# Kernel tuning notes

Hardware: AMD Instinct MI355X
Metric: run time of the kernel (lower is better)

Reference implementation:

```python
import jax, jax.numpy as jnp
import numpy as np

B, S, D, H = 8, 512, 768, 12
DH = D // H  # head size 64


def setup_inputs() -> dict:
    key = jax.random.key(0)
    ks = jax.random.split(key, 24)
    std = D ** -0.5
    w = lambda k, shape: jax.random.normal(k, shape, jnp.float32) * std
    b = lambda k, n: jax.random.normal(k, (n,), jnp.float32) * 0.01
    return {
        "hidden_states": jax.random.normal(ks[0], (B, S, D), jnp.float32),
        "mol": jax.random.normal(ks[1], (B, S, D), jnp.float32),
        "Wq": w(ks[2], (D, D)), "bq": b(ks[3], D),
        "Wk": w(ks[4], (D, D)), "bk": b(ks[5], D),
        "Wv": w(ks[6], (D, D)), "bv": b(ks[7], D),
        "Wqm": w(ks[8], (D, D)), "bqm": b(ks[9], D),
        "Wkm": w(ks[10], (D, D)), "bkm": b(ks[11], D),
        "Wvm": w(ks[12], (D, D)), "bvm": b(ks[13], D),
        "Wfc": w(ks[14], (2 * D, D)), "bfc": b(ks[15], D),
        "Wfcm": w(ks[16], (2 * D, D)), "bfcm": b(ks[17], D),
        "Wo": w(ks[18], (D, D)), "bo": b(ks[19], D),
        "Wom": w(ks[20], (D, D)), "bom": b(ks[21], D),
    }


def _split_heads(x):
    # [B,S,D] -> [B,H,S,DH]
    b_, s_, _ = x.shape
    return x.reshape(b_, s_, H, DH).transpose(0, 2, 1, 3)


def _merge_heads(x):
    # [B,H,S,DH] -> [B,S,D]
    b_, _, s_, _ = x.shape
    return x.transpose(0, 2, 1, 3).reshape(b_, s_, H * DH)


def _attend(q, k, v):
    # q:[B,H,Sq,DH], k,v:[B,H,Sk,DH]  (dropout rate = 0 -> identity)
    scores = jnp.einsum('bhqd,bhkd->bhqk', q, k) / np.sqrt(DH).astype(np.float32)
    probs = jax.nn.softmax(scores, axis=-1)
    return _merge_heads(jnp.einsum('bhqk,bhkd->bhqd', probs, v))


def reference(hidden_states, mol, Wq, bq, Wk, bk, Wv, bv, Wqm, bqm, Wkm, bkm,
              Wvm, bvm, Wfc, bfc, Wfcm, bfcm, Wo, bo, Wom, bom):
    q = _split_heads(hidden_states @ Wq + bq)
    k = _split_heads(hidden_states @ Wk + bk)
    v = _split_heads(hidden_states @ Wv + bv)
    qm = _split_heads(mol @ Wqm + bqm)
    km = _split_heads(mol @ Wkm + bkm)
    vm = _split_heads(mol @ Wvm + bvm)

    # prot branch: self-attn (q over prot K/V) + guided attn (mol Q over prot K/V)
    a_pp = _attend(q, k, v)      # [B,S,D]
    a_mp = _attend(qm, k, v)     # [B,S,D]
    attn_prot = (jnp.concatenate([a_pp, a_mp], axis=-1) @ Wfc + bfc) @ Wo + bo

    # mol branch: self-attn (mol Q over mol K/V) + guided attn (prot Q over mol K/V)
    a_mm = _attend(qm, km, vm)
    a_pm = _attend(q, km, vm)
    attn_mol = (jnp.concatenate([a_mm, a_pm], axis=-1) @ Wfcm + bfcm) @ Wom + bom

    return attn_prot, attn_mol
```

## Files before the change

kernel.cpp:

```cpp
#include <hip/hip_runtime.h>
#include <math.h>

#define B_   8
#define S_   512
#define D_   768
#define H_   12
#define DH_  64
#define NTOK (B_*S_)
#define D2_  (2*D_)
#define ND_  ((size_t)NTOK * D_)
#define WSZ_ ((size_t)D_ * D_)
#define FSZ_ ((size_t)D2_ * D_)

typedef unsigned short ushortT;
typedef short bf16x8 __attribute__((ext_vector_type(8)));
typedef float f32x4  __attribute__((ext_vector_type(4)));
typedef unsigned int u32;

#define QSCL 0.1803368801111204f

__device__ __forceinline__ unsigned short f2bf(float f) {
    unsigned int x = __float_as_uint(f);
    unsigned int lsb = (x >> 16) & 1u;
    x += 0x7fffu + lsb;
    return (unsigned short)(x >> 16);
}
__device__ __forceinline__ u32 pkbf(float a, float b) {
    u32 ua = (__float_as_uint(a) + 0x8000u) >> 16;
    u32 ub = (__float_as_uint(b) + 0x8000u) & 0xffff0000u;
    return ua | ub;
}

#if __has_builtin(__builtin_amdgcn_exp2f)
#define EXP2(x) __builtin_amdgcn_exp2f(x)
#else
#define EXP2(x) exp2f(x)
#endif

__device__ __forceinline__ void ld_g2l16(const ushortT* g, ushortT* l) {
    __builtin_amdgcn_global_load_lds(
        (const __attribute__((address_space(1))) u32*)g,
        (__attribute__((address_space(3))) u32*)l, 16, 0, 0);
}

struct CvtJob { const float* in[4]; ushortT* out[4]; int n4[4]; };
__global__ __launch_bounds__(256) void convert_bf16_k(CvtJob cj)
{
    const int z = blockIdx.z;
    int i4 = blockIdx.x * 256 + threadIdx.x;
    if (i4 >= cj.n4[z]) return;
    size_t i = (size_t)i4 * 4;
    float4 f = *(const float4*)(cj.in[z] + i);
    ushort4 u;
    u.x = f2bf(f.x); u.y = f2bf(f.y); u.z = f2bf(f.z); u.w = f2bf(f.w);
    *(ushort4*)(cj.out[z] + i) = u;
}

struct TransJob { const float* in[8]; ushortT* out[8]; float scl[8]; };
__global__ __launch_bounds__(256) void transpose_w(TransJob tj)
{
    __shared__ float t[32][33];
    const int z = blockIdx.z;
    const float* __restrict__ in = tj.in[z];
    ushortT* __restrict__ out = tj.out[z];
    const float scl = tj.scl[z];
    const int r0 = blockIdx.y * 32, c0 = blockIdx.x * 32;
    const int x = threadIdx.x & 31, y = threadIdx.x >> 5;
    #pragma unroll
    for (int i = 0; i < 4; ++i)
        t[y + 8 * i][x] = in[(size_t)(r0 + y + 8 * i) * D_ + c0 + x];
    __syncthreads();
    #pragma unroll
    for (int i = 0; i < 4; ++i)
        out[(size_t)(c0 + y + 8 * i) * D_ + r0 + x] = f2bf(t[x][y + 8 * i] * scl);
}

__global__ __launch_bounds__(256) void transpose_v(
    const ushortT* __restrict__ v, const ushortT* __restrict__ vm,
    ushortT* __restrict__ vt, ushortT* __restrict__ vmt)
{
    __shared__ ushortT t[64][65];
    const ushortT* __restrict__ in = blockIdx.z ? vm : v;
    ushortT* __restrict__ out = blockIdx.z ? vmt : vt;
    const int bh = blockIdx.y, b = bh / H_, h = bh % H_;
    const int s0 = blockIdx.x * 64;
    const int c4 = threadIdx.x & 15, r = threadIdx.x >> 4;
    #pragma unroll
    for (int i = 0; i < 4; ++i) {
        int row = r + 16 * i;
        ushort4 u = *(const ushort4*)(in + (size_t)(b * S_ + s0 + row) * D_ + h * DH_ + c4 * 4);
        t[row][c4 * 4 + 0] = u.x; t[row][c4 * 4 + 1] = u.y;
        t[row][c4 * 4 + 2] = u.z; t[row][c4 * 4 + 3] = u.w;
    }
    __syncthreads();
    #pragma unroll
    for (int i = 0; i < 4; ++i) {
        int d = r + 16 * i;
        ushort4 u;
        u.x = t[c4 * 4 + 0][d]; u.y = t[c4 * 4 + 1][d];
        u.z = t[c4 * 4 + 2][d]; u.w = t[c4 * 4 + 3][d];
        *(ushort4*)(out + (size_t)(bh * DH_ + d) * S_ + s0 + c4 * 4) = u;
    }
}

__global__ __launch_bounds__(256) void init_bco(
    const float* __restrict__ bo, const float* __restrict__ bom,
    float* __restrict__ bcoP, float* __restrict__ bcoM)
{
    int n = blockIdx.x * 256 + threadIdx.x;
    if (n < D_) { bcoP[n] = bo[n]; bcoM[n] = bom[n]; }
}
__global__ __launch_bounds__(256) void fold_bias(
    const float* __restrict__ bfc, const float* __restrict__ Wo,
    const float* __restrict__ bfcm, const float* __restrict__ Wom,
    float* __restrict__ bcoP, float* __restrict__ bcoM)
{
    const float* bf_ = blockIdx.z ? bfcm : bfc;
    const float* W_  = blockIdx.z ? Wom : Wo;
    float* o_ = blockIdx.z ? bcoM : bcoP;
    int n = blockIdx.x * 256 + threadIdx.x;
    int j0 = blockIdx.y * 96;
    float s = 0.f;
    #pragma unroll 8
    for (int j = j0; j < j0 + 96; ++j) s += bf_[j] * W_[(size_t)j * D_ + n];
    atomicAdd(&o_[n], s);
}

struct GemmJob {
    const ushortT* X[6];
    const ushortT* Wt[6];
    const float*   bias[6];
    float          bscale[6];
    void*          Y[6];
};
__global__ __launch_bounds__(256) void gemm_mfma(GemmJob gb, int K, int ldy, int flags)
{
    __shared__ __attribute__((aligned(16))) ushortT At[128 * 32];
    __shared__ __attribute__((aligned(16))) ushortT Bt[128 * 32];

    const int z = blockIdx.z;
    const ushortT* __restrict__ X  = gb.X[z];
    const ushortT* __restrict__ Wt = gb.Wt[z];
    const float* __restrict__ bias = gb.bias[z];

    const int tid = threadIdx.x;
    const int lane = tid & 63, wave = tid >> 6;
    const int quad = lane >> 4, l16 = lane & 15;
    const int wm = wave >> 1, wn = wave & 1;
    const int bm = blockIdx.y * 128, bn = blockIdx.x * 128;

    f32x4 acc[4][4];
    #pragma unroll
    for (int i = 0; i < 4; ++i)
        #pragma unroll
        for (int j = 0; j < 4; ++j)
            acc[i][j] = (f32x4){0.f, 0.f, 0.f, 0.f};

    const int c0 = tid, c1 = tid + 256;
    const int r0c = c0 >> 2, k0c = (((c0 & 3) ^ ((r0c >> 1) & 3))) * 8;
    const int r1c = c1 >> 2, k1c = (((c1 & 3) ^ ((r1c >> 1) & 3))) * 8;
    const int swl = (l16 >> 1) & 3;
    const int rdo = ((quad ^ swl)) * 8;

    for (int k0 = 0; k0 < K; k0 += 32) {
        __syncthreads();
        ld_g2l16(X  + (size_t)(bm + r0c) * K + k0 + k0c, &At[c0 * 8]);
        ld_g2l16(X  + (size_t)(bm + r1c) * K + k0 + k1c, &At[c1 * 8]);
        ld_g2l16(Wt + (size_t)(bn + r0c) * K + k0 + k0c, &Bt[c0 * 8]);
        ld_g2l16(Wt + (size_t)(bn + r1c) * K + k0 + k1c, &Bt[c1 * 8]);
        __syncthreads();

        bf16x8 af[4], bf[4];
        #pragma unroll
        for (int mt = 0; mt < 4; ++mt)
            af[mt] = *(const bf16x8*)&At[(wm * 64 + mt * 16 + l16) * 32 + rdo];
        #pragma unroll
        for (int nt = 0; nt < 4; ++nt)
            bf[nt] = *(const bf16x8*)&Bt[(wn * 64 + nt * 16 + l16) * 32 + rdo];
        #pragma unroll
        for (int mt = 0; mt < 4; ++mt)
            #pragma unroll
            for (int nt = 0; nt < 4; ++nt)
                acc[mt][nt] = __builtin_amdgcn_mfma_f32_16x16x32_bf16(af[mt], bf[nt], acc[mt][nt], 0, 0, 0);
    }

    const int row0 = bm + wm * 64, col0 = bn + wn * 64;
    #pragma unroll
    for (int mt = 0; mt < 4; ++mt) {
        #pragma unroll
        for (int nt = 0; nt < 4; ++nt) {
            const int col = col0 + nt * 16 + l16;
            const float bval = (flags & 2) ? bias[col] * gb.bscale[z] : 0.f;
            #pragma unroll
            for (int r = 0; r < 4; ++r) {
                const int row = row0 + mt * 16 + quad * 4 + r;
                float vsum = acc[mt][nt][r] + bval;
                if (flags & 1) ((float*)gb.Y[z])[(size_t)row * ldy + col] = vsum;
                else           ((ushortT*)gb.Y[z])[(size_t)row * ldy + col] = f2bf(vsum);
            }
        }
    }
}

__global__ __launch_bounds__(256) void attn_mfma(
    const ushortT* __restrict__ q,  const ushortT* __restrict__ k,
    const ushortT* __restrict__ vt, const ushortT* __restrict__ qm,
    const ushortT* __restrict__ km, const ushortT* __restrict__ vmt,
    ushortT* __restrict__ catP, ushortT* __restrict__ catM)
{
    __shared__ __attribute__((aligned(16))) ushortT Kt0[64 * 32], Kt1[64 * 32];
    __shared__ __attribute__((aligned(16))) ushortT Vt0[64 * 32], Vt1[64 * 32];
    __shared__ __attribute__((aligned(16))) ushortT Pt0[4][32 * 32], Pt1[4][32 * 32];

    const int tid = threadIdx.x;
    const int lane = tid & 63, wave = tid >> 6;
    const int quad = lane >> 4, l16 = lane & 15;
    const int bh = blockIdx.y, b = bh / H_, h = bh % H_;
    const int q0w = blockIdx.x * 128 + wave * 32;

    const ushortT *Q, *Kp, *Vp;
    ushortT* Out;
    int colbase;
    switch (blockIdx.z) {
        case 0:  Q = q;  Kp = k;  Vp = vt;  Out = catP; colbase = 0;  break;
        case 1:  Q = qm; Kp = k;  Vp = vt;  Out = catP; colbase = D_; break;
        case 2:  Q = qm; Kp = km; Vp = vmt; Out = catM; colbase = 0;  break;
        default: Q = q;  Kp = km; Vp = vmt; Out = catM; colbase = D_; break;
    }

    bf16x8 Qf[2][2];
    #pragma unroll
    for (int mt = 0; mt < 2; ++mt)
        #pragma unroll
        for (int kc = 0; kc < 2; ++kc)
            Qf[mt][kc] = *(const bf16x8*)(Q + (size_t)(b * S_ + q0w + mt * 16 + l16) * D_
                                            + h * DH_ + kc * 32 + quad * 8);

    f32x4 OT[4][2];
    #pragma unroll
    for (int dt = 0; dt < 4; ++dt)
        #pragma unroll
        for (int mt = 0; mt < 2; ++mt)
            OT[dt][mt] = (f32x4){0.f, 0.f, 0.f, 0.f};
    float lrun[2] = {0.f, 0.f};

    const int drow = tid >> 2;
    const int dcl  = ((tid & 3) ^ ((drow >> 1) & 3)) * 8;
    const ushortT* gK = Kp + (size_t)(b * S_) * D_ + h * DH_ + (size_t)drow * D_ + dcl;
    const ushortT* gV = Vp + (size_t)bh * DH_ * S_ + (size_t)drow * S_ + dcl;

    const int swl = (l16 >> 1) & 3;
    const int rdo = (quad ^ swl) * 8;
    int roff[4];
    #pragma unroll
    for (int t = 0; t < 4; ++t) roff[t] = (t * 16 + l16) * 32 + rdo;
    int wpoff[2][2];
    #pragma unroll
    for (int mt = 0; mt < 2; ++mt)
        #pragma unroll
        for (int kb = 0; kb < 2; ++kb)
            wpoff[mt][kb] = (mt * 16 + l16) * 32 + (((kb * 2 + (quad >> 1)) ^ swl) * 8) + (quad & 1) * 4;

    for (int kt = 0; kt < S_; kt += 64) {
        __syncthreads();
        ld_g2l16(gK,      &Kt0[tid * 8]);
        ld_g2l16(gK + 32, &Kt1[tid * 8]);
        ld_g2l16(gV,      &Vt0[tid * 8]);
        ld_g2l16(gV + 32, &Vt1[tid * 8]);
        gK += (size_t)64 * D_;
        gV += 64;
        __syncthreads();

        f32x4 St[4][2];
        #pragma unroll
        for (int ktl = 0; ktl < 4; ++ktl)
            #pragma unroll
            for (int mt = 0; mt < 2; ++mt)
                St[ktl][mt] = (f32x4){0.f, 0.f, 0.f, 0.f};
        #pragma unroll
        for (int ktl = 0; ktl < 4; ++ktl) {
            bf16x8 ka0 = *(const bf16x8*)&Kt0[roff[ktl]];
            bf16x8 ka1 = *(const bf16x8*)&Kt1[roff[ktl]];
            #pragma unroll
            for (int mt = 0; mt < 2; ++mt) {
                St[ktl][mt] = __builtin_amdgcn_mfma_f32_16x16x32_bf16(ka0, Qf[mt][0], St[ktl][mt], 0, 0, 0);
                St[ktl][mt] = __builtin_amdgcn_mfma_f32_16x16x32_bf16(ka1, Qf[mt][1], St[ktl][mt], 0, 0, 0);
            }
        }

        #pragma unroll
        for (int mt = 0; mt < 2; ++mt) {
            float rs = 0.f;
            #pragma unroll
            for (int ktl = 0; ktl < 4; ++ktl) {
                float p0 = EXP2(St[ktl][mt][0]);
                float p1 = EXP2(St[ktl][mt][1]);
                float p2 = EXP2(St[ktl][mt][2]);
                float p3 = EXP2(St[ktl][mt][3]);
                rs += (p0 + p1) + (p2 + p3);
                uint2 u = make_uint2(pkbf(p0, p1), pkbf(p2, p3));
                if (ktl < 2) *(uint2*)&Pt0[wave][wpoff[mt][ktl & 1]] = u;
                else         *(uint2*)&Pt1[wave][wpoff[mt][ktl & 1]] = u;
            }
            lrun[mt] += rs;
        }

        bf16x8 Pb[2][2];
        #pragma unroll
        for (int mt = 0; mt < 2; ++mt) {
            Pb[mt][0] = *(const bf16x8*)&Pt0[wave][(mt * 16 + l16) * 32 + rdo];
            Pb[mt][1] = *(const bf16x8*)&Pt1[wave][(mt * 16 + l16) * 32 + rdo];
        }
        #pragma unroll
        for (int dt = 0; dt < 4; ++dt) {
            bf16x8 va0 = *(const bf16x8*)&Vt0[roff[dt]];
            bf16x8 va1 = *(const bf16x8*)&Vt1[roff[dt]];
            #pragma unroll
            for (int mt = 0; mt < 2; ++mt) {
                OT[dt][mt] = __builtin_amdgcn_mfma_f32_16x16x32_bf16(va0, Pb[mt][0], OT[dt][mt], 0, 0, 0);
                OT[dt][mt] = __builtin_amdgcn_mfma_f32_16x16x32_bf16(va1, Pb[mt][1], OT[dt][mt], 0, 0, 0);
            }
        }
    }

    #pragma unroll
    for (int mt = 0; mt < 2; ++mt) {
        float l = lrun[mt];
        l += __shfl_xor(l, 16, 64);
        l += __shfl_xor(l, 32, 64);
        const float inv = 1.f / l;
        ushortT* yp = Out + (size_t)(b * S_ + q0w + mt * 16 + l16) * D2_ + colbase + h * DH_;
        #pragma unroll
        for (int dt = 0; dt < 4; ++dt) {
            uint2 u = make_uint2(pkbf(OT[dt][mt][0] * inv, OT[dt][mt][1] * inv),
                                 pkbf(OT[dt][mt][2] * inv, OT[dt][mt][3] * inv));
            *(uint2*)(yp + dt * 16 + quad * 4) = u;
        }
    }
}

extern "C" void kernel_launch(void* const* d_in, const int* in_sizes, int n_in,
                              void* d_out, int out_size, void* d_ws, size_t ws_size,
                              hipStream_t stream) {
    const float* hs   = (const float*)d_in[0];
    const float* mol  = (const float*)d_in[1];
    const float* Wq   = (const float*)d_in[2];
    const float* bq   = (const float*)d_in[3];
    const float* Wk   = (const float*)d_in[4];
    const float* bk   = (const float*)d_in[5];
    const float* Wv   = (const float*)d_in[6];
    const float* bv   = (const float*)d_in[7];
    const float* Wqm  = (const float*)d_in[8];
    const float* bqm  = (const float*)d_in[9];
    const float* Wkm  = (const float*)d_in[10];
    const float* bkm  = (const float*)d_in[11];
    const float* Wvm  = (const float*)d_in[12];
    const float* bvm  = (const float*)d_in[13];
    const float* Wfc  = (const float*)d_in[14];
    const float* bfc  = (const float*)d_in[15];
    const float* Wfcm = (const float*)d_in[16];
    const float* bfcm = (const float*)d_in[17];
    const float* Wo   = (const float*)d_in[18];
    const float* bo   = (const float*)d_in[19];
    const float* Wom  = (const float*)d_in[20];
    const float* bom  = (const float*)d_in[21];

    float* out = (float*)d_out;
    ushortT* ws = (ushortT*)d_ws;

    ushortT* hsb   = ws;
    ushortT* molb  = hsb + ND_;
    ushortT* Wfcb  = molb + ND_;
    ushortT* Wfcmb = Wfcb + FSZ_;
    ushortT* WqT   = Wfcmb + FSZ_;
    ushortT* WkT   = WqT + WSZ_;
    ushortT* WvT   = WkT + WSZ_;
    ushortT* WqmT  = WvT + WSZ_;
    ushortT* WkmT  = WqmT + WSZ_;
    ushortT* WvmT  = WkmT + WSZ_;
    ushortT* WoT   = WvmT + WSZ_;
    ushortT* WomT  = WoT + WSZ_;
    ushortT* WcoT  = WomT + WSZ_;
    ushortT* WcomT = WcoT + FSZ_;
    ushortT* q     = WcomT + FSZ_;
    ushortT* k     = q + ND_;
    ushortT* v     = k + ND_;
    ushortT* qm    = v + ND_;
    ushortT* km    = qm + ND_;
    ushortT* vm    = km + ND_;
    ushortT* vtr   = vm + ND_;
    ushortT* vmtr  = vtr + ND_;
    ushortT* catP  = vmtr + ND_;
    ushortT* catM  = catP + 2 * ND_;
    float*   bcoP  = (float*)(catM + 2 * ND_);
    float*   bcoM  = bcoP + D_;

    {
        CvtJob cj;
        cj.in[0] = hs;  cj.out[0] = hsb;   cj.n4[0] = (int)(ND_ / 4);
        cj.in[1] = mol; cj.out[1] = molb;  cj.n4[1] = (int)(ND_ / 4);
        cj.in[2] = Wfc; cj.out[2] = Wfcb;  cj.n4[2] = (int)(FSZ_ / 4);
        cj.in[3] = Wfcm;cj.out[3] = Wfcmb; cj.n4[3] = (int)(FSZ_ / 4);
        convert_bf16_k<<<dim3(ND_ / 1024, 1, 4), 256, 0, stream>>>(cj);
    }

    {
        TransJob tj;
        const float* wi[8] = {Wq, Wk, Wv, Wqm, Wkm, Wvm, Wo, Wom};
        ushortT* wo_[8]    = {WqT, WkT, WvT, WqmT, WkmT, WvmT, WoT, WomT};
        const float sc[8]  = {QSCL, 1.f, 1.f, QSCL, 1.f, 1.f, 1.f, 1.f};
        for (int i = 0; i < 8; ++i) { tj.in[i] = wi[i]; tj.out[i] = wo_[i]; tj.scl[i] = sc[i]; }
        transpose_w<<<dim3(D_ / 32, D_ / 32, 8), 256, 0, stream>>>(tj);
    }

    init_bco<<<dim3(3), 256, 0, stream>>>(bo, bom, bcoP, bcoM);
    fold_bias<<<dim3(3, 8, 2), 256, 0, stream>>>(bfc, Wo, bfcm, Wom, bcoP, bcoM);

    {
        GemmJob gb = {};
        gb.X[0] = WoT;  gb.Wt[0] = Wfcb;  gb.bias[0] = bcoP; gb.bscale[0] = 1.f; gb.Y[0] = WcoT;
        gb.X[1] = WomT; gb.Wt[1] = Wfcmb; gb.bias[1] = bcoM; gb.bscale[1] = 1.f; gb.Y[1] = WcomT;
        gemm_mfma<<<dim3(D2_ / 128, D_ / 128, 2), 256, 0, stream>>>(gb, D_, D2_, 0);
    }

    {
        GemmJob gb = {};
        gb.X[0] = hsb;  gb.Wt[0] = WqT;  gb.bias[0] = bq;  gb.bscale[0] = QSCL; gb.Y[0] = q;
        gb.X[1] = hsb;  gb.Wt[1] = WkT;  gb.bias[1] = bk;  gb.bscale[1] = 1.f;  gb.Y[1] = k;
        gb.X[2] = hsb;  gb.Wt[2] = WvT;  gb.bias[2] = bv;  gb.bscale[2] = 1.f;  gb.Y[2] = v;
        gb.X[3] = molb; gb.Wt[3] = WqmT; gb.bias[3] = bqm; gb.bscale[3] = QSCL; gb.Y[3] = qm;
        gb.X[4] = molb; gb.Wt[4] = WkmT; gb.bias[4] = bkm; gb.bscale[4] = 1.f;  gb.Y[4] = km;
        gb.X[5] = molb; gb.Wt[5] = WvmT; gb.bias[5] = bvm; gb.bscale[5] = 1.f;  gb.Y[5] = vm;
        gemm_mfma<<<dim3(D_ / 128, NTOK / 128, 6), 256, 0, stream>>>(gb, D_, D_, 2);
    }

    transpose_v<<<dim3(S_ / 64, B_ * H_, 2), 256, 0, stream>>>(v, vm, vtr, vmtr);

    attn_mfma<<<dim3(S_ / 128, B_ * H_, 4), 256, 0, stream>>>(q, k, vtr, qm, km, vmtr, catP, catM);

    {
        GemmJob gb = {};
        gb.X[0] = catP; gb.Wt[0] = WcoT;  gb.bias[0] = bcoP; gb.bscale[0] = 1.f; gb.Y[0] = out;
        gb.X[1] = catM; gb.Wt[1] = WcomT; gb.bias[1] = bcoM; gb.bscale[1] = 1.f; gb.Y[1] = out + ND_;
        gemm_mfma<<<dim3(D_ / 128, NTOK / 128, 2), 256, 0, stream>>>(gb, D2_, D_, 3);
    }
}
```

Before: 319.7 us.

## Merge prep kernels and fuse weight-fold GEMM with QKV GEMM; widen K tile

Merges the bf16 conversion, weight transposes and bias folding into one flat-indexed prep kernel. The bias fold becomes a single serial loop per output column instead of split atomics. The Wo·Wfc weight-fold GEMM and the six QKV projection GEMMs now run in one flattened launch with per-job tables, and the GEMM K-tile grows from 32 to 64 with a new swizzle. This cuts kernel launches and tail idle time between small grids, at the cost of double LDS per block and a serial 768-length bias loop in a few blocks.

```diff
diff --git a/kernel.cpp b/kernel.cpp
--- a/kernel.cpp
+++ b/kernel.cpp
@@ -43,36 +43,158 @@
         (__attribute__((address_space(3))) u32*)l, 16, 0, 0);
 }
 
-struct CvtJob { const float* in[4]; ushortT* out[4]; int n4[4]; };
-__global__ __launch_bounds__(256) void convert_bf16_k(CvtJob cj)
-{
-    const int z = blockIdx.z;
-    int i4 = blockIdx.x * 256 + threadIdx.x;
-    if (i4 >= cj.n4[z]) return;
-    size_t i = (size_t)i4 * 4;
-    float4 f = *(const float4*)(cj.in[z] + i);
-    ushort4 u;
-    u.x = f2bf(f.x); u.y = f2bf(f.y); u.z = f2bf(f.z); u.w = f2bf(f.w);
-    *(ushort4*)(cj.out[z] + i) = u;
-}
-
-struct TransJob { const float* in[8]; ushortT* out[8]; float scl[8]; };
-__global__ __launch_bounds__(256) void transpose_w(TransJob tj)
+#define PREP_NBLK 13062
+struct PrepJob {
+    const float *hs, *mol, *Wfc, *Wfcm;
+    ushortT *hsb, *molb, *Wfcb, *Wfcmb;
+    const float* tw_in[8]; ushortT* tw_out[8]; float tw_scl[8];
+    const float *bfc, *Wo, *bo, *bfcm, *Wom, *bom;
+    float *bcoP, *bcoM;
+};
+__global__ __launch_bounds__(256) void prep_k(PrepJob pj)
 {
     __shared__ float t[32][33];
-    const int z = blockIdx.z;
-    const float* __restrict__ in = tj.in[z];
-    ushortT* __restrict__ out = tj.out[z];
-    const float scl = tj.scl[z];
-    const int r0 = blockIdx.y * 32, c0 = blockIdx.x * 32;
-    const int x = threadIdx.x & 31, y = threadIdx.x >> 5;
+    const int bx = blockIdx.x;
+    const int tid = threadIdx.x;
+
+    if (bx < 8448) {
+        const float* in; ushortT* out; int base;
+        if (bx < 3072)      { in = pj.hs;   out = pj.hsb;   base = 0; }
+        else if (bx < 6144) { in = pj.mol;  out = pj.molb;  base = 3072; }
+        else if (bx < 7296) { in = pj.Wfc;  out = pj.Wfcb;  base = 6144; }
+        else                { in = pj.Wfcm; out = pj.Wfcmb; base = 7296; }
+        size_t i = ((size_t)(bx - base) * 256 + tid) * 4;
+        float4 f = *(const float4*)(in + i);
+        ushort4 u;
+        u.x = f2bf(f.x); u.y = f2bf(f.y); u.z = f2bf(f.z); u.w = f2bf(f.w);
+        *(ushort4*)(out + i) = u;
+    } else if (bx < 13056) {
+        int sub = bx - 8448;
+        int z = sub / 576, r = sub - z * 576;
+        int by = r / 24, bxx = r - by * 24;
+        const float* __restrict__ in = pj.tw_in[z];
+        ushortT* __restrict__ out = pj.tw_out[z];
+        const float scl = pj.tw_scl[z];
+        const int r0 = by * 32, c0 = bxx * 32;
+        const int x = tid & 31, y = tid >> 5;
+        #pragma unroll
+        for (int i = 0; i < 4; ++i)
+            t[y + 8 * i][x] = in[(size_t)(r0 + y + 8 * i) * D_ + c0 + x];
+        __syncthreads();
+        #pragma unroll
+        for (int i = 0; i < 4; ++i)
+            out[(size_t)(c0 + y + 8 * i) * D_ + r0 + x] = f2bf(t[x][y + 8 * i] * scl);
+    } else {
+        int b = bx - 13056;
+        int zb = b / 3;
+        int n = (b - zb * 3) * 256 + tid;
+        const float* bf_ = zb ? pj.bfcm : pj.bfc;
+        const float* W_  = zb ? pj.Wom : pj.Wo;
+        const float* bo_ = zb ? pj.bom : pj.bo;
+        float* o_ = zb ? pj.bcoM : pj.bcoP;
+        float s = bo_[n];
+        #pragma unroll 8
+        for (int j = 0; j < D_; ++j) s += bf_[j] * W_[(size_t)j * D_ + n];
+        o_[n] = s;
+    }
+}
+
+struct GJob {
+    const ushortT* X;
+    const ushortT* Wt;
+    const float*   bias;
+    float          bscale;
+    void*          Y;
+    int            nx;
+    int            nblk;
+    int            ldy;
+    int            flags;
+};
+struct GJobs { GJob j[8]; };
+__global__ __launch_bounds__(256) void gemm_flat(GJobs gjs, int K)
+{
+    __shared__ __attribute__((aligned(16))) ushortT At[128 * 64];
+    __shared__ __attribute__((aligned(16))) ushortT Bt[128 * 64];
+
+    int bx = blockIdx.x;
+    int ji = 0;
+    while (bx >= gjs.j[ji].nblk) { bx -= gjs.j[ji].nblk; ++ji; }
+    const ushortT* __restrict__ X  = gjs.j[ji].X;
+    const ushortT* __restrict__ Wt = gjs.j[ji].Wt;
+    const float* __restrict__ bias = gjs.j[ji].bias;
+    const float bscale = gjs.j[ji].bscale;
+    void* Y        = gjs.j[ji].Y;
+    const int nx   = gjs.j[ji].nx;
+    const int ldy  = gjs.j[ji].ldy;
+    const int flags= gjs.j[ji].flags;
+
+    const int by = bx / nx, bxx = bx - by * nx;
+    const int bm = by * 128, bn = bxx * 128;
+
+    const int tid = threadIdx.x;
+    const int lane = tid & 63, wave = tid >> 6;
+    const int quad = lane >> 4, l16 = lane & 15;
+    const int wm = wave >> 1, wn = wave & 1;
+
+    f32x4 acc[4][4];
     #pragma unroll
     for (int i = 0; i < 4; ++i)
-        t[y + 8 * i][x] = in[(size_t)(r0 + y + 8 * i) * D_ + c0 + x];
-    __syncthreads();
-    #pragma unroll
-    for (int i = 0; i < 4; ++i)
-        out[(size_t)(c0 + y + 8 * i) * D_ + r0 + x] = f2bf(t[x][y + 8 * i] * scl);
+        #pragma unroll
+        for (int j = 0; j < 4; ++j)
+            acc[i][j] = (f32x4){0.f, 0.f, 0.f, 0.f};
+
+    const int crow = tid >> 3;
+    const int cko  = ((tid & 7) ^ (crow & 7)) * 8;
+    int px[2];
+    px[0] = ((quad) ^ (l16 & 7)) * 8;
+    px[1] = ((4 + quad) ^ (l16 & 7)) * 8;
+
+    const ushortT* gX = X + (size_t)(bm + crow) * K + cko;
+    const ushortT* gW = Wt + (size_t)(bn + crow) * K + cko;
+
+    for (int k0 = 0; k0 < K; k0 += 64) {
+        __syncthreads();
+        #pragma unroll
+        for (int i = 0; i < 4; ++i) {
+            const int s = tid + i * 256;
+            ld_g2l16(gX + (size_t)(i * 32) * K + k0, &At[s * 8]);
+            ld_g2l16(gW + (size_t)(i * 32) * K + k0, &Bt[s * 8]);
+        }
+        __syncthreads();
+
+        #pragma unroll
+        for (int kc = 0; kc < 2; ++kc) {
+            bf16x8 af[4], bf[4];
+            #pragma unroll
+            for (int mt = 0; mt < 4; ++mt)
+                af[mt] = *(const bf16x8*)&At[(wm * 64 + mt * 16 + l16) * 64 + px[kc]];
+            #pragma unroll
+            for (int nt = 0; nt < 4; ++nt)
+                bf[nt] = *(const bf16x8*)&Bt[(wn * 64 + nt * 16 + l16) * 64 + px[kc]];
+            #pragma unroll
+            for (int mt = 0; mt < 4; ++mt)
+                #pragma unroll
+                for (int nt = 0; nt < 4; ++nt)
+                    acc[mt][nt] = __builtin_amdgcn_mfma_f32_16x16x32_bf16(af[mt], bf[nt], acc[mt][nt], 0, 0, 0);
+        }
+    }
+
+    const int row0 = bm + wm * 64, col0 = bn + wn * 64;
+    #pragma unroll
+    for (int mt = 0; mt < 4; ++mt) {
+        #pragma unroll
+        for (int nt = 0; nt < 4; ++nt) {
+            const int col = col0 + nt * 16 + l16;
+            const float bval = (flags & 2) ? bias[col] * bscale : 0.f;
+            #pragma unroll
+            for (int r = 0; r < 4; ++r) {
+                const int row = row0 + mt * 16 + quad * 4 + r;
+                float vsum = acc[mt][nt][r] + bval;
+                if (flags & 1) ((float*)Y)[(size_t)row * ldy + col] = vsum;
+                else           ((ushortT*)Y)[(size_t)row * ldy + col] = f2bf(vsum);
+            }
+        }
+    }
 }
 
 __global__ __launch_bounds__(256) void transpose_v(
@@ -100,105 +222,6 @@
         u.x = t[c4 * 4 + 0][d]; u.y = t[c4 * 4 + 1][d];
         u.z = t[c4 * 4 + 2][d]; u.w = t[c4 * 4 + 3][d];
         *(ushort4*)(out + (size_t)(bh * DH_ + d) * S_ + s0 + c4 * 4) = u;
-    }
-}
-
-__global__ __launch_bounds__(256) void init_bco(
-    const float* __restrict__ bo, const float* __restrict__ bom,
-    float* __restrict__ bcoP, float* __restrict__ bcoM)
-{
-    int n = blockIdx.x * 256 + threadIdx.x;
-    if (n < D_) { bcoP[n] = bo[n]; bcoM[n] = bom[n]; }
-}
-__global__ __launch_bounds__(256) void fold_bias(
-    const float* __restrict__ bfc, const float* __restrict__ Wo,
-    const float* __restrict__ bfcm, const float* __restrict__ Wom,
-    float* __restrict__ bcoP, float* __restrict__ bcoM)
-{
-    const float* bf_ = blockIdx.z ? bfcm : bfc;
-    const float* W_  = blockIdx.z ? Wom : Wo;
-    float* o_ = blockIdx.z ? bcoM : bcoP;
-    int n = blockIdx.x * 256 + threadIdx.x;
-    int j0 = blockIdx.y * 96;
-    float s = 0.f;
-    #pragma unroll 8
-    for (int j = j0; j < j0 + 96; ++j) s += bf_[j] * W_[(size_t)j * D_ + n];
-    atomicAdd(&o_[n], s);
-}
-
-struct GemmJob {
-    const ushortT* X[6];
-    const ushortT* Wt[6];
-    const float*   bias[6];
-    float          bscale[6];
-    void*          Y[6];
-};
-__global__ __launch_bounds__(256) void gemm_mfma(GemmJob gb, int K, int ldy, int flags)
-{
-    __shared__ __attribute__((aligned(16))) ushortT At[128 * 32];
-    __shared__ __attribute__((aligned(16))) ushortT Bt[128 * 32];
-
-    const int z = blockIdx.z;
-    const ushortT* __restrict__ X  = gb.X[z];
-    const ushortT* __restrict__ Wt = gb.Wt[z];
-    const float* __restrict__ bias = gb.bias[z];
-
-    const int tid = threadIdx.x;
-    const int lane = tid & 63, wave = tid >> 6;
-    const int quad = lane >> 4, l16 = lane & 15;
-    const int wm = wave >> 1, wn = wave & 1;
-    const int bm = blockIdx.y * 128, bn = blockIdx.x * 128;
-
-    f32x4 acc[4][4];
-    #pragma unroll
-    for (int i = 0; i < 4; ++i)
-        #pragma unroll
-        for (int j = 0; j < 4; ++j)
-            acc[i][j] = (f32x4){0.f, 0.f, 0.f, 0.f};
-
-    const int c0 = tid, c1 = tid + 256;
-    const int r0c = c0 >> 2, k0c = (((c0 & 3) ^ ((r0c >> 1) & 3))) * 8;
-    const int r1c = c1 >> 2, k1c = (((c1 & 3) ^ ((r1c >> 1) & 3))) * 8;
-    const int swl = (l16 >> 1) & 3;
-    const int rdo = ((quad ^ swl)) * 8;
-
-    for (int k0 = 0; k0 < K; k0 += 32) {
-        __syncthreads();
-        ld_g2l16(X  + (size_t)(bm + r0c) * K + k0 + k0c, &At[c0 * 8]);
-        ld_g2l16(X  + (size_t)(bm + r1c) * K + k0 + k1c, &At[c1 * 8]);
-        ld_g2l16(Wt + (size_t)(bn + r0c) * K + k0 + k0c, &Bt[c0 * 8]);
-        ld_g2l16(Wt + (size_t)(bn + r1c) * K + k0 + k1c, &Bt[c1 * 8]);
-        __syncthreads();
-
-        bf16x8 af[4], bf[4];
-        #pragma unroll
-        for (int mt = 0; mt < 4; ++mt)
-            af[mt] = *(const bf16x8*)&At[(wm * 64 + mt * 16 + l16) * 32 + rdo];
-        #pragma unroll
-        for (int nt = 0; nt < 4; ++nt)
-            bf[nt] = *(const bf16x8*)&Bt[(wn * 64 + nt * 16 + l16) * 32 + rdo];
-        #pragma unroll
-        for (int mt = 0; mt < 4; ++mt)
-            #pragma unroll
-            for (int nt = 0; nt < 4; ++nt)
-                acc[mt][nt] = __builtin_amdgcn_mfma_f32_16x16x32_bf16(af[mt], bf[nt], acc[mt][nt], 0, 0, 0);
-    }
-
-    const int row0 = bm + wm * 64, col0 = bn + wn * 64;
-    #pragma unroll
-    for (int mt = 0; mt < 4; ++mt) {
-        #pragma unroll
-        for (int nt = 0; nt < 4; ++nt) {
-            const int col = col0 + nt * 16 + l16;
-            const float bval = (flags & 2) ? bias[col] * gb.bscale[z] : 0.f;
-            #pragma unroll
-            for (int r = 0; r < 4; ++r) {
-                const int row = row0 + mt * 16 + quad * 4 + r;
-                float vsum = acc[mt][nt][r] + bval;
-                if (flags & 1) ((float*)gb.Y[z])[(size_t)row * ldy + col] = vsum;
-                else           ((ushortT*)gb.Y[z])[(size_t)row * ldy + col] = f2bf(vsum);
-            }
-        }
     }
 }
 
@@ -396,52 +419,39 @@
     float*   bcoM  = bcoP + D_;
 
     {
-        CvtJob cj;
-        cj.in[0] = hs;  cj.out[0] = hsb;   cj.n4[0] = (int)(ND_ / 4);
-        cj.in[1] = mol; cj.out[1] = molb;  cj.n4[1] = (int)(ND_ / 4);
-        cj.in[2] = Wfc; cj.out[2] = Wfcb;  cj.n4[2] = (int)(FSZ_ / 4);
-        cj.in[3] = Wfcm;cj.out[3] = Wfcmb; cj.n4[3] = (int)(FSZ_ / 4);
-        convert_bf16_k<<<dim3(ND_ / 1024, 1, 4), 256, 0, stream>>>(cj);
-    }
-
-    {
-        TransJob tj;
+        PrepJob pj;
+        pj.hs = hs; pj.mol = mol; pj.Wfc = Wfc; pj.Wfcm = Wfcm;
+        pj.hsb = hsb; pj.molb = molb; pj.Wfcb = Wfcb; pj.Wfcmb = Wfcmb;
         const float* wi[8] = {Wq, Wk, Wv, Wqm, Wkm, Wvm, Wo, Wom};
         ushortT* wo_[8]    = {WqT, WkT, WvT, WqmT, WkmT, WvmT, WoT, WomT};
         const float sc[8]  = {QSCL, 1.f, 1.f, QSCL, 1.f, 1.f, 1.f, 1.f};
-        for (int i = 0; i < 8; ++i) { tj.in[i] = wi[i]; tj.out[i] = wo_[i]; tj.scl[i] = sc[i]; }
-        transpose_w<<<dim3(D_ / 32, D_ / 32, 8), 256, 0, stream>>>(tj);
-    }
-
-    init_bco<<<dim3(3), 256, 0, stream>>>(bo, bom, bcoP, bcoM);
-    fold_bias<<<dim3(3, 8, 2), 256, 0, stream>>>(bfc, Wo, bfcm, Wom, bcoP, bcoM);
+        for (int i = 0; i < 8; ++i) { pj.tw_in[i] = wi[i]; pj.tw_out[i] = wo_[i]; pj.tw_scl[i] = sc[i]; }
+        pj.bfc = bfc; pj.Wo = Wo; pj.bo = bo; pj.bfcm = bfcm; pj.Wom = Wom; pj.bom = bom;
+        pj.bcoP = bcoP; pj.bcoM = bcoM;
+        prep_k<<<dim3(PREP_NBLK), 256, 0, stream>>>(pj);
+    }
 
     {
-        GemmJob gb = {};
-        gb.X[0] = WoT;  gb.Wt[0] = Wfcb;  gb.bias[0] = bcoP; gb.bscale[0] = 1.f; gb.Y[0] = WcoT;
-        gb.X[1] = WomT; gb.Wt[1] = Wfcmb; gb.bias[1] = bcoM; gb.bscale[1] = 1.f; gb.Y[1] = WcomT;
-        gemm_mfma<<<dim3(D2_ / 128, D_ / 128, 2), 256, 0, stream>>>(gb, D_, D2_, 0);
-    }
+        GJobs gj = {};
+        gj.j[0] = {WoT,  Wfcb,  nullptr, 1.f,  WcoT,  12, 72,  D2_, 0};
+        gj.j[1] = {WomT, Wfcmb, nullptr, 1.f,  WcomT, 12, 72,  D2_, 0};
+        gj.j[2] = {hsb,  WqT,  bq,  QSCL, q,  6, 192, D_, 2};
+        gj.j[3] = {hsb,  WkT,  bk,  1.f,  k,  6, 192, D_, 2};
+        gj.j[4] = {hsb,  WvT,  bv,  1.f,  v,  6, 192, D_, 2};
+        gj.j[5] = {molb, WqmT, bqm, QSCL, qm, 6, 192, D_, 2};
+        gj.j[6] = {molb, WkmT, bkm, 1.f,  km, 6, 192, D_, 2};
+        gj.j[7] = {molb, WvmT, bvm, 1.f,  vm, 6, 192, D_, 2};
+        gemm_flat<<<dim3(72 * 2 + 192 * 6), 256, 0, stream>>>(gj, D_);
+    }
+
+    transpose_v<<<dim3(S_ / 64, B_ * H_, 2), 256, 0, stream>>>(v, vm, vtr, vmtr);
+
+    attn_mfma<<<dim3(S_ / 128, B_ * H_, 4), 256, 0, stream>>>(q, k, vtr, qm, km, vmtr, catP, catM);
 
     {
-        GemmJob gb = {};
-        gb.X[0] = hsb;  gb.Wt[0] = WqT;  gb.bias[0] = bq;  gb.bscale[0] = QSCL; gb.Y[0] = q;
-        gb.X[1] = hsb;  gb.Wt[1] = WkT;  gb.bias[1] = bk;  gb.bscale[1] = 1.f;  gb.Y[1] = k;
-        gb.X[2] = hsb;  gb.Wt[2] = WvT;  gb.bias[2] = bv;  gb.bscale[2] = 1.f;  gb.Y[2] = v;
-        gb.X[3] = molb; gb.Wt[3] = WqmT; gb.bias[3] = bqm; gb.bscale[3] = QSCL; gb.Y[3] = qm;
-        gb.X[4] = molb; gb.Wt[4] = WkmT; gb.bias[4] = bkm; gb.bscale[4] = 1.f;  gb.Y[4] = km;
-        gb.X[5] = molb; gb.Wt[5] = WvmT; gb.bias[5] = bvm; gb.bscale[5] = 1.f;  gb.Y[5] = vm;
-        gemm_mfma<<<dim3(D_ / 128, NTOK / 128, 6), 256, 0, stream>>>(gb, D_, D_, 2);
-    }
-
-    transpose_v<<<dim3(S_ / 64, B_ * H_, 2), 256, 0, stream>>>(v, vm, vtr, vmtr);
-
-    attn_mfma<<<dim3(S_ / 128, B_ * H_, 4), 256, 0, stream>>>(q, k, vtr, qm, km, vmtr, catP, catM);
-
-    {
-        GemmJob gb = {};
-        gb.X[0] = catP; gb.Wt[0] = WcoT;  gb.bias[0] = bcoP; gb.bscale[0] = 1.f; gb.Y[0] = out;
-        gb.X[1] = catM; gb.Wt[1] = WcomT; gb.bias[1] = bcoM; gb.bscale[1] = 1.f; gb.Y[1] = out + ND_;
-        gemm_mfma<<<dim3(D_ / 128, NTOK / 128, 2), 256, 0, stream>>>(gb, D2_, D_, 3);
-    }
-}
+        GJobs gj = {};
+        gj.j[0] = {catP, WcoT,  bcoP, 1.f, out,       6, 192, D_, 3};
+        gj.j[1] = {catM, WcomT, bcoM, 1.f, out + ND_, 6, 192, D_, 3};
+        gemm_flat<<<dim3(192 * 2), 256, 0, stream>>>(gj, D2_);
+    }
+}
```

Result: faster. 302.8 us (-5.3%).
